# Performance work log

Measured on AMD Instinct MI355X. Metric: run time of the kernel, lower is better.

The kernel has to match this reference:

```python
import jax, jax.numpy as jnp
import numpy as np

N = 100000   # nodes
E = 1600000  # edges
IN = 128     # in_dim
H = 128      # hidden
C = 9        # num_classes
G = 256      # graphs in batch


def setup_inputs() -> dict:
    key = jax.random.key(0)
    ks = jax.random.split(key, 24)
    w = lambda k, shp: jax.random.normal(k, shp, dtype=jnp.float32) * 0.05
    inp = {
        "x": jax.random.normal(ks[0], (N, IN), dtype=jnp.float32),
        "edge_index": jax.random.randint(ks[1], (2, E), 0, N, dtype=jnp.int32),
        "batch": jnp.sort(jax.random.randint(ks[2], (N,), 0, G, dtype=jnp.int32)),
        # GIN layer 0 MLP: Linear(IN,H) -> ReLU -> Linear(H,H)
        "l0_w1": w(ks[3], (IN, H)), "l0_b1": jnp.zeros((H,), jnp.float32),
        "l0_w2": w(ks[4], (H, H)),  "l0_b2": jnp.zeros((H,), jnp.float32),
        # GIN layer 1 MLP
        "l1_w1": w(ks[5], (H, H)), "l1_b1": jnp.zeros((H,), jnp.float32),
        "l1_w2": w(ks[6], (H, H)), "l1_b2": jnp.zeros((H,), jnp.float32),
        # GlobalAttention gate: Linear(H,1)
        "gate_w": w(ks[7], (H, 1)), "gate_b": jnp.zeros((1,), jnp.float32),
        # classification head: Linear(H,H) -> ReLU -> Linear(H,C)
        "cls_w1": w(ks[8], (H, H)), "cls_b1": jnp.zeros((H,), jnp.float32),
        "cls_w2": w(ks[9], (H, C)), "cls_b2": jnp.zeros((C,), jnp.float32),
        "reg_w1": w(ks[10], (H, H)), "reg_b1": jnp.zeros((H,), jnp.float32),
        "reg_w2": w(ks[11], (H, 1)), "reg_b2": jnp.zeros((1,), jnp.float32),
    }
    return inp


def reference(x, edge_index, batch,
              l0_w1, l0_b1, l0_w2, l0_b2,
              l1_w1, l1_b1, l1_w2, l1_b2,
              gate_w, gate_b,
              cls_w1, cls_b1, cls_w2, cls_b2,
              reg_w1, reg_b1, reg_w2, reg_b2):
    src, dst = edge_index[0], edge_index[1]

    def gin_layer(h, w1, b1, w2, b2):
        # GINConv with eps=0: (1+eps)*h + sum_{j in N(i)} h_j, then MLP, then outer ReLU
        agg = jax.ops.segment_sum(h[src], dst, num_segments=N)
        z = h + agg
        z = jax.nn.relu(z @ w1 + b1) @ w2 + b2
        return jax.nn.relu(z)

    h = gin_layer(x, l0_w1, l0_b1, l0_w2, l0_b2)
    h = gin_layer(h, l1_w1, l1_b1, l1_w2, l1_b2)

    # GlobalAttention readout: per-graph segment softmax over gate scores
    gate = (h @ gate_w + gate_b)[:, 0]                      # [N]
    m = jax.ops.segment_max(gate, batch, num_segments=G)    # [G]
    a = jnp.exp(gate - m[batch])                            # [N]
    denom = jax.ops.segment_sum(a, batch, num_segments=G)   # [G]
    wgt = a / denom[batch]                                  # [N]
    g = jax.ops.segment_sum(h * wgt[:, None], batch, num_segments=G)  # [G, H]

    cls = jax.nn.relu(g @ cls_w1 + cls_b1) @ cls_w2 + cls_b2
    reg = jax.nn.relu(g @ reg_w1 + reg_b1) @ reg_w2 + reg_b2
    return cls, reg
```

## Files before the change

### kernel.cpp

```cpp
#include <hip/hip_runtime.h>

#define N_NODES 100000
#define N_EDGES 1600000
#define HDIM    128
#define NGRAPH  256
#define NRES    8
#define PAD     64

typedef __attribute__((ext_vector_type(8))) short short8;
typedef __attribute__((ext_vector_type(4))) float f32x4;

__device__ inline ushort f32_to_bf16_rtne(float x) {
    uint u = __builtin_bit_cast(uint, x);
    uint r = u + 0x7FFFu + ((u >> 16) & 1u);
    return (ushort)(r >> 16);
}
__device__ inline float bf16_to_f32(ushort h) {
    return __builtin_bit_cast(float, (uint)h << 16);
}

__global__ __launch_bounds__(256) void scatter_pad_kernel(
        const int* __restrict__ src, const int* __restrict__ dst,
        int* __restrict__ cnt, int* __restrict__ eadj, int E) {
    int res  = blockIdx.x & (NRES - 1);
    int grp  = blockIdx.x >> 3;
    int ngrp = gridDim.x >> 3;
    int lo = res * (N_NODES / NRES), hi = lo + (N_NODES / NRES);
    for (int e = grp * 256 + threadIdx.x; e < E; e += ngrp * 256) {
        int d = dst[e];
        if (d >= lo && d < hi) {
            int p = atomicAdd(&cnt[d], 1);
            if (p < PAD) eadj[(size_t)d * PAD + p] = src[e];
        }
    }
}

__global__ __launch_bounds__(256) void f2b_kernel(const float* __restrict__ x,
                                                  ushort* __restrict__ xb, int n4) {
    for (int i = blockIdx.x * 256 + threadIdx.x; i < n4; i += gridDim.x * 256) {
        float4 v = ((const float4*)x)[i];
        ushort4 o;
        o.x = f32_to_bf16_rtne(v.x); o.y = f32_to_bf16_rtne(v.y);
        o.z = f32_to_bf16_rtne(v.z); o.w = f32_to_bf16_rtne(v.w);
        ((ushort4*)xb)[i] = o;
    }
}

__global__ void pack4_kernel(const float* __restrict__ wa, const float* __restrict__ wb,
                             const float* __restrict__ wc, const float* __restrict__ wd,
                             ushort* __restrict__ ha, ushort* __restrict__ la,
                             ushort* __restrict__ hb, ushort* __restrict__ lb,
                             ushort* __restrict__ hc, ushort* __restrict__ lc,
                             ushort* __restrict__ hd, ushort* __restrict__ ld) {
    int sel = blockIdx.x >> 6;
    const float* w = sel == 0 ? wa : sel == 1 ? wb : sel == 2 ? wc : wd;
    ushort* hi = sel == 0 ? ha : sel == 1 ? hb : sel == 2 ? hc : hd;
    ushort* lo = sel == 0 ? la : sel == 1 ? lb : sel == 2 ? lc : ld;
    int t = (blockIdx.x & 63) * 256 + threadIdx.x;
    int i = t & 7, lane = (t >> 3) & 63, cfg = (t >> 9) & 7, ks = t >> 12;
    int k = ks * 32 + (lane >> 4) * 8 + i;
    int c = cfg * 16 + (lane & 15);
    float v = w[k * 128 + c];
    ushort h = f32_to_bf16_rtne(v);
    hi[t] = h;
    lo[t] = f32_to_bf16_rtne(v - bf16_to_f32(h));
}

template<bool LAST>
__global__ __launch_bounds__(256, 8) void gin_layer_kernel(
        const ushort* __restrict__ hbin,
        const int* __restrict__ cnt, const int* __restrict__ eadj,
        const ushort* __restrict__ w1h, const ushort* __restrict__ w1l,
        const float* __restrict__ b1,
        const ushort* __restrict__ w2h, const ushort* __restrict__ w2l,
        const float* __restrict__ b2,
        ushort* __restrict__ hbout,
        const float* __restrict__ gw, const float* __restrict__ gb,
        float* __restrict__ gateb) {
    __shared__ ushort zh[32 * 128];
    __shared__ ushort zl[32 * 128];
    int tid  = threadIdx.x;
    int lane = tid & 63;
    int wv   = tid >> 6;
    int row0 = blockIdx.x * 32;
    int cfg0 = wv * 2;
    int lrow = lane & 15;
    int lhi  = lane >> 4;
    const ushort2* hb2 = (const ushort2*)hbin;

    for (int j = 0; j < 4; j++) {
        int lrA = wv + 4 * j, lrB = lrA + 16;
        int rowA = row0 + lrA, rowB = row0 + lrB;
        float ax = 0.f, ay = 0.f, bx = 0.f, by = 0.f;
        int dA = 0, dB = 0;
        if (rowA < N_NODES) {
            ushort2 s = hb2[(size_t)rowA * 64 + lane];
            ax = bf16_to_f32(s.x); ay = bf16_to_f32(s.y);
            dA = cnt[rowA]; dA = dA > PAD ? PAD : dA;
        }
        if (rowB < N_NODES) {
            ushort2 s = hb2[(size_t)rowB * 64 + lane];
            bx = bf16_to_f32(s.x); by = bf16_to_f32(s.y);
            dB = cnt[rowB]; dB = dB > PAD ? PAD : dB;
        }
        const int* eA = eadj + (size_t)rowA * PAD;
        const int* eB = eadj + (size_t)rowB * PAD;
        int ia = 0, ib = 0;
        while (ia + 4 <= dA && ib + 4 <= dB) {
            int sa0 = eA[ia], sa1 = eA[ia + 1], sa2 = eA[ia + 2], sa3 = eA[ia + 3];
            int sb0 = eB[ib], sb1 = eB[ib + 1], sb2 = eB[ib + 2], sb3 = eB[ib + 3];
            ushort2 va0 = hb2[(size_t)sa0 * 64 + lane], va1 = hb2[(size_t)sa1 * 64 + lane];
            ushort2 va2 = hb2[(size_t)sa2 * 64 + lane], va3 = hb2[(size_t)sa3 * 64 + lane];
            ushort2 vb0 = hb2[(size_t)sb0 * 64 + lane], vb1 = hb2[(size_t)sb1 * 64 + lane];
            ushort2 vb2 = hb2[(size_t)sb2 * 64 + lane], vb3 = hb2[(size_t)sb3 * 64 + lane];
            ax += bf16_to_f32(va0.x) + bf16_to_f32(va1.x) + bf16_to_f32(va2.x) + bf16_to_f32(va3.x);
            ay += bf16_to_f32(va0.y) + bf16_to_f32(va1.y) + bf16_to_f32(va2.y) + bf16_to_f32(va3.y);
            bx += bf16_to_f32(vb0.x) + bf16_to_f32(vb1.x) + bf16_to_f32(vb2.x) + bf16_to_f32(vb3.x);
            by += bf16_to_f32(vb0.y) + bf16_to_f32(vb1.y) + bf16_to_f32(vb2.y) + bf16_to_f32(vb3.y);
            ia += 4; ib += 4;
        }
        while (ia + 4 <= dA) {
            int s0 = eA[ia], s1 = eA[ia + 1], s2 = eA[ia + 2], s3 = eA[ia + 3];
            ushort2 v0 = hb2[(size_t)s0 * 64 + lane], v1 = hb2[(size_t)s1 * 64 + lane];
            ushort2 v2 = hb2[(size_t)s2 * 64 + lane], v3 = hb2[(size_t)s3 * 64 + lane];
            ax += bf16_to_f32(v0.x) + bf16_to_f32(v1.x) + bf16_to_f32(v2.x) + bf16_to_f32(v3.x);
            ay += bf16_to_f32(v0.y) + bf16_to_f32(v1.y) + bf16_to_f32(v2.y) + bf16_to_f32(v3.y);
            ia += 4;
        }
        while (ib + 4 <= dB) {
            int s0 = eB[ib], s1 = eB[ib + 1], s2 = eB[ib + 2], s3 = eB[ib + 3];
            ushort2 v0 = hb2[(size_t)s0 * 64 + lane], v1 = hb2[(size_t)s1 * 64 + lane];
            ushort2 v2 = hb2[(size_t)s2 * 64 + lane], v3 = hb2[(size_t)s3 * 64 + lane];
            bx += bf16_to_f32(v0.x) + bf16_to_f32(v1.x) + bf16_to_f32(v2.x) + bf16_to_f32(v3.x);
            by += bf16_to_f32(v0.y) + bf16_to_f32(v1.y) + bf16_to_f32(v2.y) + bf16_to_f32(v3.y);
            ib += 4;
        }
        for (; ia < dA; ia++) {
            ushort2 v = hb2[(size_t)eA[ia] * 64 + lane];
            ax += bf16_to_f32(v.x); ay += bf16_to_f32(v.y);
        }
        for (; ib < dB; ib++) {
            ushort2 v = hb2[(size_t)eB[ib] * 64 + lane];
            bx += bf16_to_f32(v.x); by += bf16_to_f32(v.y);
        }
        {
            ushort h0 = f32_to_bf16_rtne(ax); ushort l0 = f32_to_bf16_rtne(ax - bf16_to_f32(h0));
            ushort h1 = f32_to_bf16_rtne(ay); ushort l1 = f32_to_bf16_rtne(ay - bf16_to_f32(h1));
            int off = (lrA * 256 + lane * 4) ^ ((lrA & 7) << 4);
            *(ushort2*)((char*)zh + off) = make_ushort2(h0, h1);
            *(ushort2*)((char*)zl + off) = make_ushort2(l0, l1);
        }
        {
            ushort h0 = f32_to_bf16_rtne(bx); ushort l0 = f32_to_bf16_rtne(bx - bf16_to_f32(h0));
            ushort h1 = f32_to_bf16_rtne(by); ushort l1 = f32_to_bf16_rtne(by - bf16_to_f32(h1));
            int off = (lrB * 256 + lane * 4) ^ ((lrB & 7) << 4);
            *(ushort2*)((char*)zh + off) = make_ushort2(h0, h1);
            *(ushort2*)((char*)zl + off) = make_ushort2(l0, l1);
        }
    }
    __syncthreads();

    f32x4 acc[2][2];
    #pragma unroll
    for (int rf = 0; rf < 2; rf++)
        #pragma unroll
        for (int cf = 0; cf < 2; cf++) acc[rf][cf] = (f32x4){0.f, 0.f, 0.f, 0.f};

    for (int ks = 0; ks < 4; ks++) {
        short8 bh[2], bl[2];
        #pragma unroll
        for (int cf = 0; cf < 2; cf++) {
            size_t bidx = (((size_t)ks * 8 + cfg0 + cf) * 64 + lane) * 8;
            bh[cf] = *(const short8*)&w1h[bidx];
            bl[cf] = *(const short8*)&w1l[bidx];
        }
        #pragma unroll
        for (int rf = 0; rf < 2; rf++) {
            int r = rf * 16 + lrow;
            int off = (r * 256 + ks * 64 + lhi * 16) ^ ((r & 7) << 4);
            short8 ah = *(const short8*)((const char*)zh + off);
            short8 al = *(const short8*)((const char*)zl + off);
            #pragma unroll
            for (int cf = 0; cf < 2; cf++) {
                acc[rf][cf] = __builtin_amdgcn_mfma_f32_16x16x32_bf16(ah, bh[cf], acc[rf][cf], 0, 0, 0);
                acc[rf][cf] = __builtin_amdgcn_mfma_f32_16x16x32_bf16(al, bh[cf], acc[rf][cf], 0, 0, 0);
                acc[rf][cf] = __builtin_amdgcn_mfma_f32_16x16x32_bf16(ah, bl[cf], acc[rf][cf], 0, 0, 0);
            }
        }
    }
    __syncthreads();

    #pragma unroll
    for (int cf = 0; cf < 2; cf++) {
        int c = (cfg0 + cf) * 16 + lrow;
        float bias = b1[c];
        #pragma unroll
        for (int rf = 0; rf < 2; rf++) {
            #pragma unroll
            for (int i = 0; i < 4; i++) {
                int r = rf * 16 + lhi * 4 + i;
                float v = fmaxf(acc[rf][cf][i] + bias, 0.f);
                ushort h = f32_to_bf16_rtne(v);
                ushort l = f32_to_bf16_rtne(v - bf16_to_f32(h));
                int off = (r * 256 + c * 2) ^ ((r & 7) << 4);
                *(ushort*)((char*)zh + off) = h;
                *(ushort*)((char*)zl + off) = l;
            }
        }
    }
    __syncthreads();

    #pragma unroll
    for (int rf = 0; rf < 2; rf++)
        #pragma unroll
        for (int cf = 0; cf < 2; cf++) acc[rf][cf] = (f32x4){0.f, 0.f, 0.f, 0.f};

    for (int ks = 0; ks < 4; ks++) {
        short8 bh[2], bl[2];
        #pragma unroll
        for (int cf = 0; cf < 2; cf++) {
            size_t bidx = (((size_t)ks * 8 + cfg0 + cf) * 64 + lane) * 8;
            bh[cf] = *(const short8*)&w2h[bidx];
            bl[cf] = *(const short8*)&w2l[bidx];
        }
        #pragma unroll
        for (int rf = 0; rf < 2; rf++) {
            int r = rf * 16 + lrow;
            int off = (r * 256 + ks * 64 + lhi * 16) ^ ((r & 7) << 4);
            short8 ah = *(const short8*)((const char*)zh + off);
            short8 al = *(const short8*)((const char*)zl + off);
            #pragma unroll
            for (int cf = 0; cf < 2; cf++) {
                acc[rf][cf] = __builtin_amdgcn_mfma_f32_16x16x32_bf16(ah, bh[cf], acc[rf][cf], 0, 0, 0);
                acc[rf][cf] = __builtin_amdgcn_mfma_f32_16x16x32_bf16(al, bh[cf], acc[rf][cf], 0, 0, 0);
                acc[rf][cf] = __builtin_amdgcn_mfma_f32_16x16x32_bf16(ah, bl[cf], acc[rf][cf], 0, 0, 0);
            }
        }
    }

    float pg[8];
    if (LAST) {
        #pragma unroll
        for (int q = 0; q < 8; q++) pg[q] = 0.f;
    }
    #pragma unroll
    for (int cf = 0; cf < 2; cf++) {
        int c = (cfg0 + cf) * 16 + lrow;
        float bias = b2[c];
        float gwc = LAST ? gw[c] : 0.f;
        #pragma unroll
        for (int rf = 0; rf < 2; rf++) {
            #pragma unroll
            for (int i = 0; i < 4; i++) {
                int row = row0 + rf * 16 + lhi * 4 + i;
                float v = fmaxf(acc[rf][cf][i] + bias, 0.f);
                if (row < N_NODES) hbout[(size_t)row * 128 + c] = f32_to_bf16_rtne(v);
                if (LAST) pg[rf * 4 + i] += v * gwc;
            }
        }
    }
    if (LAST) {
        #pragma unroll
        for (int off = 1; off < 16; off <<= 1)
            #pragma unroll
            for (int q = 0; q < 8; q++) pg[q] += __shfl_xor(pg[q], off);
        __syncthreads();
        float* gpart = (float*)zh;
        if (lrow == 0) {
            #pragma unroll
            for (int rf = 0; rf < 2; rf++)
                #pragma unroll
                for (int i = 0; i < 4; i++)
                    gpart[wv * 32 + rf * 16 + lhi * 4 + i] = pg[rf * 4 + i];
        }
        __syncthreads();
        if (tid < 32) {
            int row = row0 + tid;
            if (row < N_NODES)
                gateb[row] = gpart[tid] + gpart[32 + tid] + gpart[64 + tid] + gpart[96 + tid] + gb[0];
        }
    }
}

__device__ inline int lower_bound_i(const int* a, int n, int v) {
    int lo = 0, hi = n;
    while (lo < hi) {
        int mid = (lo + hi) >> 1;
        if (a[mid] < v) lo = mid + 1; else hi = mid;
    }
    return lo;
}

__global__ __launch_bounds__(512) void readout_kernel(
        const ushort* __restrict__ h2b, const float* __restrict__ gate,
        const int* __restrict__ batch,
        const float* __restrict__ cw1, const float* __restrict__ cb1,
        const float* __restrict__ cw2, const float* __restrict__ cb2,
        const float* __restrict__ rw1, const float* __restrict__ rb1,
        const float* __restrict__ rw2, const float* __restrict__ rb2,
        float* __restrict__ out) {
    int g = blockIdx.x, t = threadIdx.x;
    int wv = t >> 6, lane = t & 63;
    __shared__ int   bounds[2];
    __shared__ float red[512];
    __shared__ float part[8][128];
    __shared__ float gv[128];
    __shared__ float t1c[128], t1r[128];
    if (t == 0) {
        bounds[0] = lower_bound_i(batch, N_NODES, g);
        bounds[1] = lower_bound_i(batch, N_NODES, g + 1);
    }
    __syncthreads();
    int s = bounds[0], e = bounds[1];

    float m = -3.4e38f;
    for (int i = s + t; i < e; i += 512) m = fmaxf(m, gate[i]);
    red[t] = m;
    __syncthreads();
    for (int off = 256; off; off >>= 1) {
        if (t < off) red[t] = fmaxf(red[t], red[t + off]);
        __syncthreads();
    }
    m = red[0];
    __syncthreads();

    float dsum = 0.f;
    for (int i = s + t; i < e; i += 512) dsum += expf(gate[i] - m);
    red[t] = dsum;
    __syncthreads();
    for (int off = 256; off; off >>= 1) {
        if (t < off) red[t] += red[t + off];
        __syncthreads();
    }
    float denom = red[0];
    float invd = (e > s && denom > 0.f) ? 1.f / denom : 0.f;

    const ushort2* h2 = (const ushort2*)h2b;
    float a0 = 0.f, a1 = 0.f, b0 = 0.f, b1v = 0.f;
    int i0 = s + wv;
    for (; i0 + 8 < e; i0 += 16) {
        float w0 = expf(gate[i0] - m);
        float w1 = expf(gate[i0 + 8] - m);
        ushort2 v0 = h2[(size_t)i0 * 64 + lane];
        ushort2 v1 = h2[(size_t)(i0 + 8) * 64 + lane];
        a0 += w0 * bf16_to_f32(v0.x); a1 += w0 * bf16_to_f32(v0.y);
        b0 += w1 * bf16_to_f32(v1.x); b1v += w1 * bf16_to_f32(v1.y);
    }
    if (i0 < e) {
        float w0 = expf(gate[i0] - m);
        ushort2 v0 = h2[(size_t)i0 * 64 + lane];
        a0 += w0 * bf16_to_f32(v0.x); a1 += w0 * bf16_to_f32(v0.y);
    }
    part[wv][lane * 2]     = a0 + b0;
    part[wv][lane * 2 + 1] = a1 + b1v;
    __syncthreads();
    if (t < 128) {
        float acc = 0.f;
        #pragma unroll
        for (int w = 0; w < 8; w++) acc += part[w][t];
        gv[t] = acc * invd;
    }
    __syncthreads();

    if (t < 128) {
        float a = cb1[t];
        for (int k = 0; k < HDIM; k++) a += gv[k] * cw1[k * HDIM + t];
        t1c[t] = fmaxf(a, 0.f);
    } else if (t < 256) {
        int tf = t - 128;
        float a = rb1[tf];
        for (int k = 0; k < HDIM; k++) a += gv[k] * rw1[k * HDIM + tf];
        t1r[tf] = fmaxf(a, 0.f);
    }
    __syncthreads();

    if (t < 9) {
        float acc2 = cb2[t];
        for (int k = 0; k < HDIM; k++) acc2 += t1c[k] * cw2[k * 9 + t];
        out[g * 9 + t] = acc2;
    }
    if (t == 64) {
        float acc2 = rb2[0];
        for (int k = 0; k < HDIM; k++) acc2 += t1r[k] * rw2[k];
        out[NGRAPH * 9 + g] = acc2;
    }
}

extern "C" void kernel_launch(void* const* d_in, const int* in_sizes, int n_in,
                              void* d_out, int out_size, void* d_ws, size_t ws_size,
                              hipStream_t stream) {
    const float* x     = (const float*)d_in[0];
    const int*   ei    = (const int*)d_in[1];
    const int*   batch = (const int*)d_in[2];
    const float *l0w1 = (const float*)d_in[3],  *l0b1 = (const float*)d_in[4];
    const float *l0w2 = (const float*)d_in[5],  *l0b2 = (const float*)d_in[6];
    const float *l1w1 = (const float*)d_in[7],  *l1b1 = (const float*)d_in[8];
    const float *l1w2 = (const float*)d_in[9],  *l1b2 = (const float*)d_in[10];
    const float *gw   = (const float*)d_in[11], *gb   = (const float*)d_in[12];
    const float *cw1  = (const float*)d_in[13], *cb1  = (const float*)d_in[14];
    const float *cw2  = (const float*)d_in[15], *cb2  = (const float*)d_in[16];
    const float *rw1  = (const float*)d_in[17], *rb1  = (const float*)d_in[18];
    const float *rw2  = (const float*)d_in[19], *rb2  = (const float*)d_in[20];
    const int* src = ei;
    const int* dst = ei + N_EDGES;
    float* out = (float*)d_out;

    char* ws = (char*)d_ws;
    size_t o = 0;
    auto alloc = [&](size_t bytes) { void* p = ws + o; o = (o + bytes + 255) & ~(size_t)255; return p; };
    ushort* h2b   = (ushort*)alloc((size_t)N_NODES * HDIM * 2);
    ushort* xb    = h2b;
    ushort* h1b   = (ushort*)alloc((size_t)N_NODES * HDIM * 2);
    int*    eadj  = (int*)alloc((size_t)N_NODES * PAD * 4);
    int*    cnt   = (int*)alloc(N_NODES * 4);
    float*  gateb = (float*)alloc(N_NODES * 4);
    ushort* w0h1 = (ushort*)alloc(16384 * 2), *w0l1 = (ushort*)alloc(16384 * 2);
    ushort* w0h2 = (ushort*)alloc(16384 * 2), *w0l2 = (ushort*)alloc(16384 * 2);
    ushort* w1h1 = (ushort*)alloc(16384 * 2), *w1l1 = (ushort*)alloc(16384 * 2);
    ushort* w1h2 = (ushort*)alloc(16384 * 2), *w1l2 = (ushort*)alloc(16384 * 2);
    (void)ws_size; (void)in_sizes; (void)n_in; (void)out_size;

    pack4_kernel<<<256, 256, 0, stream>>>(l0w1, l0w2, l1w1, l1w2,
                                          w0h1, w0l1, w0h2, w0l2,
                                          w1h1, w1l1, w1h2, w1l2);

    hipMemsetAsync(cnt, 0, N_NODES * 4, stream);
    scatter_pad_kernel<<<2048, 256, 0, stream>>>(src, dst, cnt, eadj, N_EDGES);
    f2b_kernel<<<1024, 256, 0, stream>>>(x, xb, N_NODES * HDIM / 4);

    const int layerBlocks = (N_NODES + 31) / 32;
    gin_layer_kernel<false><<<layerBlocks, 256, 0, stream>>>(
        xb, cnt, eadj, w0h1, w0l1, l0b1, w0h2, w0l2, l0b2,
        h1b, gw, gb, nullptr);
    gin_layer_kernel<true><<<layerBlocks, 256, 0, stream>>>(
        h1b, cnt, eadj, w1h1, w1l1, l1b1, w1h2, w1l2, l1b2,
        h2b, gw, gb, gateb);

    readout_kernel<<<NGRAPH, 512, 0, stream>>>(h2b, gateb, batch,
                                               cw1, cb1, cw2, cb2,
                                               rw1, rb1, rw2, rb2, out);
}
```

Before: 295.7 us.

## Switch activations to fp16 with packed-half aggregation and two-pass MFMA

Moves the stored activations and the MFMA inputs from bf16 to fp16. Neighbour aggregation is restructured so that each wave handles one row at a time, with lanes gathering 16-byte chunks from four neighbours at once and summing them with packed half2 adds and cross-lane shuffles. The activation is kept as a single fp16 operand instead of a hi/lo split, so each GEMM step issues two MFMAs instead of three and the LDS footprint and conversion work shrink. In exchange the sums are accumulated in fp16, which risks precision loss and overflow on high-degree nodes, and there is no row bound check on the last block.

```diff
diff --git a/kernel.cpp b/kernel.cpp
--- a/kernel.cpp
+++ b/kernel.cpp
@@ -1,4 +1,5 @@
 #include <hip/hip_runtime.h>
+#include <hip/hip_fp16.h>
 
 #define N_NODES 100000
 #define N_EDGES 1600000
@@ -8,16 +9,15 @@
 #define PAD     64
 
 typedef __attribute__((ext_vector_type(8))) short short8;
+typedef __attribute__((ext_vector_type(8))) _Float16 half8;
 typedef __attribute__((ext_vector_type(4))) float f32x4;
 
-__device__ inline ushort f32_to_bf16_rtne(float x) {
-    uint u = __builtin_bit_cast(uint, x);
-    uint r = u + 0x7FFFu + ((u >> 16) & 1u);
-    return (ushort)(r >> 16);
-}
-__device__ inline float bf16_to_f32(ushort h) {
-    return __builtin_bit_cast(float, (uint)h << 16);
-}
+__device__ inline uint pkadd(uint a, uint b) {
+    __half2 r = __hadd2(__builtin_bit_cast(__half2, a), __builtin_bit_cast(__half2, b));
+    return __builtin_bit_cast(uint, r);
+}
+__device__ inline ushort f2h(float x) { return __half_as_ushort(__float2half_rn(x)); }
+__device__ inline float h2f(ushort h) { return __half2float(__ushort_as_half(h)); }
 
 __global__ __launch_bounds__(256) void scatter_pad_kernel(
         const int* __restrict__ src, const int* __restrict__ dst,
@@ -30,19 +30,18 @@
         int d = dst[e];
         if (d >= lo && d < hi) {
             int p = atomicAdd(&cnt[d], 1);
-            if (p < PAD) eadj[(size_t)d * PAD + p] = src[e];
-        }
-    }
-}
-
-__global__ __launch_bounds__(256) void f2b_kernel(const float* __restrict__ x,
-                                                  ushort* __restrict__ xb, int n4) {
+            if (p < PAD) eadj[d * PAD + p] = src[e];
+        }
+    }
+}
+
+__global__ __launch_bounds__(256) void f2h_kernel(const float* __restrict__ x,
+                                                  ushort* __restrict__ xh, int n4) {
     for (int i = blockIdx.x * 256 + threadIdx.x; i < n4; i += gridDim.x * 256) {
         float4 v = ((const float4*)x)[i];
         ushort4 o;
-        o.x = f32_to_bf16_rtne(v.x); o.y = f32_to_bf16_rtne(v.y);
-        o.z = f32_to_bf16_rtne(v.z); o.w = f32_to_bf16_rtne(v.w);
-        ((ushort4*)xb)[i] = o;
+        o.x = f2h(v.x); o.y = f2h(v.y); o.z = f2h(v.z); o.w = f2h(v.w);
+        ((ushort4*)xh)[i] = o;
     }
 }
 
@@ -61,101 +60,60 @@
     int k = ks * 32 + (lane >> 4) * 8 + i;
     int c = cfg * 16 + (lane & 15);
     float v = w[k * 128 + c];
-    ushort h = f32_to_bf16_rtne(v);
+    ushort h = f2h(v);
     hi[t] = h;
-    lo[t] = f32_to_bf16_rtne(v - bf16_to_f32(h));
+    lo[t] = f2h(v - h2f(h));
 }
 
 template<bool LAST>
 __global__ __launch_bounds__(256, 8) void gin_layer_kernel(
-        const ushort* __restrict__ hbin,
+        const ushort* __restrict__ hin,
         const int* __restrict__ cnt, const int* __restrict__ eadj,
         const ushort* __restrict__ w1h, const ushort* __restrict__ w1l,
         const float* __restrict__ b1,
         const ushort* __restrict__ w2h, const ushort* __restrict__ w2l,
         const float* __restrict__ b2,
-        ushort* __restrict__ hbout,
+        ushort* __restrict__ hout,
         const float* __restrict__ gw, const float* __restrict__ gb,
         float* __restrict__ gateb) {
-    __shared__ ushort zh[32 * 128];
-    __shared__ ushort zl[32 * 128];
+    __shared__ ushort zt[32 * 128];
+    __shared__ ushort tt[32 * 128];
     int tid  = threadIdx.x;
     int lane = tid & 63;
     int wv   = tid >> 6;
     int row0 = blockIdx.x * 32;
     int cfg0 = wv * 2;
-    int lrow = lane & 15;
-    int lhi  = lane >> 4;
-    const ushort2* hb2 = (const ushort2*)hbin;
-
-    for (int j = 0; j < 4; j++) {
-        int lrA = wv + 4 * j, lrB = lrA + 16;
-        int rowA = row0 + lrA, rowB = row0 + lrB;
-        float ax = 0.f, ay = 0.f, bx = 0.f, by = 0.f;
-        int dA = 0, dB = 0;
-        if (rowA < N_NODES) {
-            ushort2 s = hb2[(size_t)rowA * 64 + lane];
-            ax = bf16_to_f32(s.x); ay = bf16_to_f32(s.y);
-            dA = cnt[rowA]; dA = dA > PAD ? PAD : dA;
-        }
-        if (rowB < N_NODES) {
-            ushort2 s = hb2[(size_t)rowB * 64 + lane];
-            bx = bf16_to_f32(s.x); by = bf16_to_f32(s.y);
-            dB = cnt[rowB]; dB = dB > PAD ? PAD : dB;
-        }
-        const int* eA = eadj + (size_t)rowA * PAD;
-        const int* eB = eadj + (size_t)rowB * PAD;
-        int ia = 0, ib = 0;
-        while (ia + 4 <= dA && ib + 4 <= dB) {
-            int sa0 = eA[ia], sa1 = eA[ia + 1], sa2 = eA[ia + 2], sa3 = eA[ia + 3];
-            int sb0 = eB[ib], sb1 = eB[ib + 1], sb2 = eB[ib + 2], sb3 = eB[ib + 3];
-            ushort2 va0 = hb2[(size_t)sa0 * 64 + lane], va1 = hb2[(size_t)sa1 * 64 + lane];
-            ushort2 va2 = hb2[(size_t)sa2 * 64 + lane], va3 = hb2[(size_t)sa3 * 64 + lane];
-            ushort2 vb0 = hb2[(size_t)sb0 * 64 + lane], vb1 = hb2[(size_t)sb1 * 64 + lane];
-            ushort2 vb2 = hb2[(size_t)sb2 * 64 + lane], vb3 = hb2[(size_t)sb3 * 64 + lane];
-            ax += bf16_to_f32(va0.x) + bf16_to_f32(va1.x) + bf16_to_f32(va2.x) + bf16_to_f32(va3.x);
-            ay += bf16_to_f32(va0.y) + bf16_to_f32(va1.y) + bf16_to_f32(va2.y) + bf16_to_f32(va3.y);
-            bx += bf16_to_f32(vb0.x) + bf16_to_f32(vb1.x) + bf16_to_f32(vb2.x) + bf16_to_f32(vb3.x);
-            by += bf16_to_f32(vb0.y) + bf16_to_f32(vb1.y) + bf16_to_f32(vb2.y) + bf16_to_f32(vb3.y);
-            ia += 4; ib += 4;
-        }
-        while (ia + 4 <= dA) {
-            int s0 = eA[ia], s1 = eA[ia + 1], s2 = eA[ia + 2], s3 = eA[ia + 3];
-            ushort2 v0 = hb2[(size_t)s0 * 64 + lane], v1 = hb2[(size_t)s1 * 64 + lane];
-            ushort2 v2 = hb2[(size_t)s2 * 64 + lane], v3 = hb2[(size_t)s3 * 64 + lane];
-            ax += bf16_to_f32(v0.x) + bf16_to_f32(v1.x) + bf16_to_f32(v2.x) + bf16_to_f32(v3.x);
-            ay += bf16_to_f32(v0.y) + bf16_to_f32(v1.y) + bf16_to_f32(v2.y) + bf16_to_f32(v3.y);
-            ia += 4;
-        }
-        while (ib + 4 <= dB) {
-            int s0 = eB[ib], s1 = eB[ib + 1], s2 = eB[ib + 2], s3 = eB[ib + 3];
-            ushort2 v0 = hb2[(size_t)s0 * 64 + lane], v1 = hb2[(size_t)s1 * 64 + lane];
-            ushort2 v2 = hb2[(size_t)s2 * 64 + lane], v3 = hb2[(size_t)s3 * 64 + lane];
-            bx += bf16_to_f32(v0.x) + bf16_to_f32(v1.x) + bf16_to_f32(v2.x) + bf16_to_f32(v3.x);
-            by += bf16_to_f32(v0.y) + bf16_to_f32(v1.y) + bf16_to_f32(v2.y) + bf16_to_f32(v3.y);
-            ib += 4;
-        }
-        for (; ia < dA; ia++) {
-            ushort2 v = hb2[(size_t)eA[ia] * 64 + lane];
-            ax += bf16_to_f32(v.x); ay += bf16_to_f32(v.y);
-        }
-        for (; ib < dB; ib++) {
-            ushort2 v = hb2[(size_t)eB[ib] * 64 + lane];
-            bx += bf16_to_f32(v.x); by += bf16_to_f32(v.y);
-        }
-        {
-            ushort h0 = f32_to_bf16_rtne(ax); ushort l0 = f32_to_bf16_rtne(ax - bf16_to_f32(h0));
-            ushort h1 = f32_to_bf16_rtne(ay); ushort l1 = f32_to_bf16_rtne(ay - bf16_to_f32(h1));
-            int off = (lrA * 256 + lane * 4) ^ ((lrA & 7) << 4);
-            *(ushort2*)((char*)zh + off) = make_ushort2(h0, h1);
-            *(ushort2*)((char*)zl + off) = make_ushort2(l0, l1);
-        }
-        {
-            ushort h0 = f32_to_bf16_rtne(bx); ushort l0 = f32_to_bf16_rtne(bx - bf16_to_f32(h0));
-            ushort h1 = f32_to_bf16_rtne(by); ushort l1 = f32_to_bf16_rtne(by - bf16_to_f32(h1));
-            int off = (lrB * 256 + lane * 4) ^ ((lrB & 7) << 4);
-            *(ushort2*)((char*)zh + off) = make_ushort2(h0, h1);
-            *(ushort2*)((char*)zl + off) = make_ushort2(l0, l1);
+    int g    = lane >> 4;
+    int q    = lane & 15;
+    const uint4* h4 = (const uint4*)hin;
+
+    for (int j = 0; j < 8; j++) {
+        int lr  = wv * 8 + j;
+        int row = row0 + lr;
+        int deg = cnt[row]; deg = deg > PAD ? PAD : deg;
+        int al  = (lane < deg) ? eadj[row * PAD + lane] : 0;
+        uint4 acc = make_uint4(0u, 0u, 0u, 0u);
+        int nch = (deg + 4) >> 2;
+        for (int c = 0; c < nch; c++) {
+            int jj = 4 * c + g - 1;
+            int nb = __shfl(al, jj < 0 ? 0 : jj);
+            int idx = jj < 0 ? row : nb;
+            if (jj < deg) {
+                uint4 u = h4[idx * 16 + q];
+                acc.x = pkadd(acc.x, u.x); acc.y = pkadd(acc.y, u.y);
+                acc.z = pkadd(acc.z, u.z); acc.w = pkadd(acc.w, u.w);
+            }
+        }
+        #pragma unroll
+        for (int off = 16; off <= 32; off <<= 1) {
+            acc.x = pkadd(acc.x, (uint)__shfl_xor((int)acc.x, off));
+            acc.y = pkadd(acc.y, (uint)__shfl_xor((int)acc.y, off));
+            acc.z = pkadd(acc.z, (uint)__shfl_xor((int)acc.z, off));
+            acc.w = pkadd(acc.w, (uint)__shfl_xor((int)acc.w, off));
+        }
+        if (g == 0) {
+            int boff = (lr * 256 + q * 16) ^ ((lr & 7) << 4);
+            *(uint4*)((char*)zt + boff) = acc;
         }
     }
     __syncthreads();
@@ -167,44 +125,38 @@
         for (int cf = 0; cf < 2; cf++) acc[rf][cf] = (f32x4){0.f, 0.f, 0.f, 0.f};
 
     for (int ks = 0; ks < 4; ks++) {
-        short8 bh[2], bl[2];
+        half8 bh[2], bl[2];
         #pragma unroll
         for (int cf = 0; cf < 2; cf++) {
-            size_t bidx = (((size_t)ks * 8 + cfg0 + cf) * 64 + lane) * 8;
-            bh[cf] = *(const short8*)&w1h[bidx];
-            bl[cf] = *(const short8*)&w1l[bidx];
+            int bidx = (((ks * 8 + cfg0 + cf) * 64 + lane) * 8);
+            bh[cf] = __builtin_bit_cast(half8, *(const short8*)&w1h[bidx]);
+            bl[cf] = __builtin_bit_cast(half8, *(const short8*)&w1l[bidx]);
         }
         #pragma unroll
         for (int rf = 0; rf < 2; rf++) {
-            int r = rf * 16 + lrow;
-            int off = (r * 256 + ks * 64 + lhi * 16) ^ ((r & 7) << 4);
-            short8 ah = *(const short8*)((const char*)zh + off);
-            short8 al = *(const short8*)((const char*)zl + off);
+            int r = rf * 16 + q;
+            int off = (r * 256 + ks * 64 + g * 16) ^ ((r & 7) << 4);
+            half8 a = __builtin_bit_cast(half8, *(const short8*)((const char*)zt + off));
             #pragma unroll
             for (int cf = 0; cf < 2; cf++) {
-                acc[rf][cf] = __builtin_amdgcn_mfma_f32_16x16x32_bf16(ah, bh[cf], acc[rf][cf], 0, 0, 0);
-                acc[rf][cf] = __builtin_amdgcn_mfma_f32_16x16x32_bf16(al, bh[cf], acc[rf][cf], 0, 0, 0);
-                acc[rf][cf] = __builtin_amdgcn_mfma_f32_16x16x32_bf16(ah, bl[cf], acc[rf][cf], 0, 0, 0);
-            }
-        }
-    }
-    __syncthreads();
+                acc[rf][cf] = __builtin_amdgcn_mfma_f32_16x16x32_f16(a, bh[cf], acc[rf][cf], 0, 0, 0);
+                acc[rf][cf] = __builtin_amdgcn_mfma_f32_16x16x32_f16(a, bl[cf], acc[rf][cf], 0, 0, 0);
+            }
+        }
+    }
 
     #pragma unroll
     for (int cf = 0; cf < 2; cf++) {
-        int c = (cfg0 + cf) * 16 + lrow;
+        int c = (cfg0 + cf) * 16 + q;
         float bias = b1[c];
         #pragma unroll
         for (int rf = 0; rf < 2; rf++) {
             #pragma unroll
             for (int i = 0; i < 4; i++) {
-                int r = rf * 16 + lhi * 4 + i;
+                int r = rf * 16 + g * 4 + i;
                 float v = fmaxf(acc[rf][cf][i] + bias, 0.f);
-                ushort h = f32_to_bf16_rtne(v);
-                ushort l = f32_to_bf16_rtne(v - bf16_to_f32(h));
                 int off = (r * 256 + c * 2) ^ ((r & 7) << 4);
-                *(ushort*)((char*)zh + off) = h;
-                *(ushort*)((char*)zl + off) = l;
+                *(ushort*)((char*)tt + off) = f2h(v);
             }
         }
     }
@@ -216,24 +168,22 @@
         for (int cf = 0; cf < 2; cf++) acc[rf][cf] = (f32x4){0.f, 0.f, 0.f, 0.f};
 
     for (int ks = 0; ks < 4; ks++) {
-        short8 bh[2], bl[2];
+        half8 bh[2], bl[2];
         #pragma unroll
         for (int cf = 0; cf < 2; cf++) {
-            size_t bidx = (((size_t)ks * 8 + cfg0 + cf) * 64 + lane) * 8;
-            bh[cf] = *(const short8*)&w2h[bidx];
-            bl[cf] = *(const short8*)&w2l[bidx];
+            int bidx = (((ks * 8 + cfg0 + cf) * 64 + lane) * 8);
+            bh[cf] = __builtin_bit_cast(half8, *(const short8*)&w2h[bidx]);
+            bl[cf] = __builtin_bit_cast(half8, *(const short8*)&w2l[bidx]);
         }
         #pragma unroll
         for (int rf = 0; rf < 2; rf++) {
-            int r = rf * 16 + lrow;
-            int off = (r * 256 + ks * 64 + lhi * 16) ^ ((r & 7) << 4);
-            short8 ah = *(const short8*)((const char*)zh + off);
-            short8 al = *(const short8*)((const char*)zl + off);
+            int r = rf * 16 + q;
+            int off = (r * 256 + ks * 64 + g * 16) ^ ((r & 7) << 4);
+            half8 a = __builtin_bit_cast(half8, *(const short8*)((const char*)tt + off));
             #pragma unroll
             for (int cf = 0; cf < 2; cf++) {
-                acc[rf][cf] = __builtin_amdgcn_mfma_f32_16x16x32_bf16(ah, bh[cf], acc[rf][cf], 0, 0, 0);
-                acc[rf][cf] = __builtin_amdgcn_mfma_f32_16x16x32_bf16(al, bh[cf], acc[rf][cf], 0, 0, 0);
-                acc[rf][cf] = __builtin_amdgcn_mfma_f32_16x16x32_bf16(ah, bl[cf], acc[rf][cf], 0, 0, 0);
+                acc[rf][cf] = __builtin_amdgcn_mfma_f32_16x16x32_f16(a, bh[cf], acc[rf][cf], 0, 0, 0);
+                acc[rf][cf] = __builtin_amdgcn_mfma_f32_16x16x32_f16(a, bl[cf], acc[rf][cf], 0, 0, 0);
             }
         }
     }
@@ -241,20 +191,20 @@
     float pg[8];
     if (LAST) {
         #pragma unroll
-        for (int q = 0; q < 8; q++) pg[q] = 0.f;
+        for (int p = 0; p < 8; p++) pg[p] = 0.f;
     }
     #pragma unroll
     for (int cf = 0; cf < 2; cf++) {
-        int c = (cfg0 + cf) * 16 + lrow;
+        int c = (cfg0 + cf) * 16 + q;
         float bias = b2[c];
         float gwc = LAST ? gw[c] : 0.f;
         #pragma unroll
         for (int rf = 0; rf < 2; rf++) {
             #pragma unroll
             for (int i = 0; i < 4; i++) {
-                int row = row0 + rf * 16 + lhi * 4 + i;
+                int row = row0 + rf * 16 + g * 4 + i;
                 float v = fmaxf(acc[rf][cf][i] + bias, 0.f);
-                if (row < N_NODES) hbout[(size_t)row * 128 + c] = f32_to_bf16_rtne(v);
+                if (row < N_NODES) hout[(size_t)row * 128 + c] = f2h(v);
                 if (LAST) pg[rf * 4 + i] += v * gwc;
             }
         }
@@ -263,15 +213,15 @@
         #pragma unroll
         for (int off = 1; off < 16; off <<= 1)
             #pragma unroll
-            for (int q = 0; q < 8; q++) pg[q] += __shfl_xor(pg[q], off);
+            for (int p = 0; p < 8; p++) pg[p] += __shfl_xor(pg[p], off);
         __syncthreads();
-        float* gpart = (float*)zh;
-        if (lrow == 0) {
+        float* gpart = (float*)zt;
+        if (q == 0) {
             #pragma unroll
             for (int rf = 0; rf < 2; rf++)
                 #pragma unroll
                 for (int i = 0; i < 4; i++)
-                    gpart[wv * 32 + rf * 16 + lhi * 4 + i] = pg[rf * 4 + i];
+                    gpart[wv * 32 + rf * 16 + g * 4 + i] = pg[rf * 4 + i];
         }
         __syncthreads();
         if (tid < 32) {
@@ -292,7 +242,7 @@
 }
 
 __global__ __launch_bounds__(512) void readout_kernel(
-        const ushort* __restrict__ h2b, const float* __restrict__ gate,
+        const ushort* __restrict__ h2h, const float* __restrict__ gate,
         const int* __restrict__ batch,
         const float* __restrict__ cw1, const float* __restrict__ cb1,
         const float* __restrict__ cw2, const float* __restrict__ cb2,
@@ -335,21 +285,21 @@
     float denom = red[0];
     float invd = (e > s && denom > 0.f) ? 1.f / denom : 0.f;
 
-    const ushort2* h2 = (const ushort2*)h2b;
+    const uint* h2u = (const uint*)h2h;
     float a0 = 0.f, a1 = 0.f, b0 = 0.f, b1v = 0.f;
     int i0 = s + wv;
     for (; i0 + 8 < e; i0 += 16) {
         float w0 = expf(gate[i0] - m);
         float w1 = expf(gate[i0 + 8] - m);
-        ushort2 v0 = h2[(size_t)i0 * 64 + lane];
-        ushort2 v1 = h2[(size_t)(i0 + 8) * 64 + lane];
-        a0 += w0 * bf16_to_f32(v0.x); a1 += w0 * bf16_to_f32(v0.y);
-        b0 += w1 * bf16_to_f32(v1.x); b1v += w1 * bf16_to_f32(v1.y);
+        __half2 v0 = __builtin_bit_cast(__half2, h2u[(size_t)i0 * 64 + lane]);
+        __half2 v1 = __builtin_bit_cast(__half2, h2u[(size_t)(i0 + 8) * 64 + lane]);
+        a0 += w0 * __low2float(v0); a1 += w0 * __high2float(v0);
+        b0 += w1 * __low2float(v1); b1v += w1 * __high2float(v1);
     }
     if (i0 < e) {
         float w0 = expf(gate[i0] - m);
-        ushort2 v0 = h2[(size_t)i0 * 64 + lane];
-        a0 += w0 * bf16_to_f32(v0.x); a1 += w0 * bf16_to_f32(v0.y);
+        __half2 v0 = __builtin_bit_cast(__half2, h2u[(size_t)i0 * 64 + lane]);
+        a0 += w0 * __low2float(v0); a1 += w0 * __high2float(v0);
     }
     part[wv][lane * 2]     = a0 + b0;
     part[wv][lane * 2 + 1] = a1 + b1v;
@@ -408,9 +358,9 @@
     char* ws = (char*)d_ws;
     size_t o = 0;
     auto alloc = [&](size_t bytes) { void* p = ws + o; o = (o + bytes + 255) & ~(size_t)255; return p; };
-    ushort* h2b   = (ushort*)alloc((size_t)N_NODES * HDIM * 2);
-    ushort* xb    = h2b;
-    ushort* h1b   = (ushort*)alloc((size_t)N_NODES * HDIM * 2);
+    ushort* h2h   = (ushort*)alloc((size_t)N_NODES * HDIM * 2);
+    ushort* xh    = h2h;
+    ushort* h1h   = (ushort*)alloc((size_t)N_NODES * HDIM * 2);
     int*    eadj  = (int*)alloc((size_t)N_NODES * PAD * 4);
     int*    cnt   = (int*)alloc(N_NODES * 4);
     float*  gateb = (float*)alloc(N_NODES * 4);
@@ -426,17 +376,17 @@
 
     hipMemsetAsync(cnt, 0, N_NODES * 4, stream);
     scatter_pad_kernel<<<2048, 256, 0, stream>>>(src, dst, cnt, eadj, N_EDGES);
-    f2b_kernel<<<1024, 256, 0, stream>>>(x, xb, N_NODES * HDIM / 4);
+    f2h_kernel<<<1024, 256, 0, stream>>>(x, xh, N_NODES * HDIM / 4);
 
     const int layerBlocks = (N_NODES + 31) / 32;
     gin_layer_kernel<false><<<layerBlocks, 256, 0, stream>>>(
-        xb, cnt, eadj, w0h1, w0l1, l0b1, w0h2, w0l2, l0b2,
-        h1b, gw, gb, nullptr);
+        xh, cnt, eadj, w0h1, w0l1, l0b1, w0h2, w0l2, l0b2,
+        h1h, gw, gb, nullptr);
     gin_layer_kernel<true><<<layerBlocks, 256, 0, stream>>>(
-        h1b, cnt, eadj, w1h1, w1l1, l1b1, w1h2, w1l2, l1b2,
-        h2b, gw, gb, gateb);
-
-    readout_kernel<<<NGRAPH, 512, 0, stream>>>(h2b, gateb, batch,
+        h1h, cnt, eadj, w1h1, w1l1, l1b1, w1h2, w1l2, l1b2,
+        h2h, gw, gb, gateb);
+
+    readout_kernel<<<NGRAPH, 512, 0, stream>>>(h2h, gateb, batch,
                                                cw1, cb1, cw2, cb2,
                                                rw1, rb1, rw2, rb2, out);
 }
```

New measurement: 282.1 us. -4.6%, faster.
